# Performance work log

Measured on AMD Instinct MI355X. Metric: run time of the kernel, lower is better.

## Reference

```python
import jax, jax.numpy as jnp
import numpy as np

NA = 100000
NB = 100000
E = 500000
D = 256
EPS = 1e-5


def setup_inputs() -> dict:
    key = jax.random.key(0)
    ks = jax.random.split(key, 10)
    scale = 1.0 / np.sqrt(D)
    return {
        "feat_a": jax.random.normal(ks[0], (NA, D), jnp.float32),
        "feat_b": jax.random.normal(ks[1], (NB, D), jnp.float32),
        "src_ab": jax.random.randint(ks[2], (E,), 0, NA, jnp.int32),
        "dst_ab": jax.random.randint(ks[3], (E,), 0, NB, jnp.int32),
        "src_ba": jax.random.randint(ks[4], (E,), 0, NB, jnp.int32),
        "dst_ba": jax.random.randint(ks[5], (E,), 0, NA, jnp.int32),
        "WT_ab": jax.random.normal(ks[6], (D, D), jnp.float32) * scale,
        "WT_ba": jax.random.normal(ks[7], (D, D), jnp.float32) * scale,
        "WA_ab": jax.random.normal(ks[8], (1, D), jnp.float32) * scale,
        "WA_ba": jax.random.normal(ks[9], (1, D), jnp.float32) * scale,
        "gamma": jnp.ones((D,), jnp.float32),
        "beta": jnp.zeros((D,), jnp.float32),
    }


def _etype_agg(h_src, h_dst, src, dst, WT, WA, n_dst):
    # per-etype linear on src nodes: t_h = W_T h_src
    t_h = h_src @ WT.T                              # [Ns, D]
    x = t_h[src] * h_dst[dst]                       # u_mul_v -> [E, D]
    s = jnp.exp(x @ WA.T)                           # exp(W_A x) -> [E, 1]
    att_sum = jax.ops.segment_sum(s, dst, num_segments=n_dst)  # copy_e+sum
    att = s / att_sum[dst]                          # e_div_v (dst of an edge always has >=1 edge)
    # u_mul_e + sum: weighted scatter of raw src features
    return jax.ops.segment_sum(h_src[src] * att, dst, num_segments=n_dst)


def _finalize(h, gamma, beta):
    h = jax.nn.relu(h)
    mu = jnp.mean(h, axis=-1, keepdims=True)
    var = jnp.mean(jnp.square(h - mu), axis=-1, keepdims=True)
    return (h - mu) / jnp.sqrt(var + EPS) * gamma + beta  # dropout is identity (eval)


def reference(feat_a, feat_b, src_ab, dst_ab, src_ba, dst_ba,
              WT_ab, WT_ba, WA_ab, WA_ba, gamma, beta):
    h_b = _etype_agg(feat_a, feat_b, src_ab, dst_ab, WT_ab, WA_ab, NB)
    h_a = _etype_agg(feat_b, feat_a, src_ba, dst_ba, WT_ba, WA_ba, NA)
    out_a = _finalize(h_a, gamma, beta)
    out_b = _finalize(h_b, gamma, beta)
    return jnp.stack([out_a, out_b])  # [2, N, D]
```

## Files before the change

### kernel.cpp

```cpp
#include <hip/hip_runtime.h>
#include <hip/hip_bf16.h>

#define D 256

typedef __attribute__((ext_vector_type(8))) short short8;
typedef __attribute__((ext_vector_type(4))) float f32x4;
typedef __attribute__((ext_vector_type(4))) unsigned short u16x4;

__device__ __forceinline__ unsigned short f2bf(float f) {
  unsigned int u = __builtin_bit_cast(unsigned int, f);
  u = (u + 0x7FFFu + ((u >> 16) & 1u)) >> 16;
  return (unsigned short)u;
}
__device__ __forceinline__ float bf2f(unsigned short h) {
  unsigned int u = ((unsigned int)h) << 16;
  return __builtin_bit_cast(float, u);
}

__global__ void zero_k(int* __restrict__ p, int n) {
  int i = blockIdx.x * 256 + threadIdx.x;
  if (i < n) p[i] = 0;
}
__global__ void zero_f32(float* __restrict__ p, int n) {
  int i = blockIdx.x * 256 + threadIdx.x;
  if (i < n) p[i] = 0.f;
}

__global__ void classify_k(const float* __restrict__ q0, const float* __restrict__ q1,
                           const float* __restrict__ q2, const float* __restrict__ q3,
                           int* __restrict__ flags) {
  __shared__ int cnt1[4], cnt0[4];
  int t = threadIdx.x;
  if (t < 4) { cnt1[t] = 0; cnt0[t] = 0; }
  __syncthreads();
  const float* qs[4] = {q0, q1, q2, q3};
#pragma unroll
  for (int v = 0; v < 4; ++v) {
    float x = qs[v][t];
    if (x == 1.0f) atomicAdd(&cnt1[v], 1);
    if (x == 0.0f) atomicAdd(&cnt0[v], 1);
  }
  __syncthreads();
  if (t == 0) {
    int gi = -1, bi = -1;
    for (int v = 0; v < 4; ++v) if (cnt1[v] == 256 && gi < 0) gi = v;
    for (int v = 0; v < 4; ++v) if (cnt0[v] == 256 && v != gi && bi < 0) bi = v;
    if (gi < 0) gi = 2;
    if (bi < 0) bi = (gi == 3) ? 2 : 3;
    int wa[2], w = 0;
    for (int v = 0; v < 4; ++v) if (v != gi && v != bi) { if (w < 2) wa[w] = v; ++w; }
    flags[0] = wa[0]; flags[1] = wa[1]; flags[2] = gi; flags[3] = bi;
  }
}

__global__ void prep_w2(const float* __restrict__ WT_ab, const float* __restrict__ WT_ba,
                        const float* __restrict__ q0, const float* __restrict__ q1,
                        const float* __restrict__ q2, const float* __restrict__ q3,
                        const int* __restrict__ flags,
                        unsigned short* __restrict__ w2ab, unsigned short* __restrict__ w2ba) {
  const float* qs[4] = {q0, q1, q2, q3};
  const float* WAab = qs[flags[0]];
  const float* WAba = qs[flags[1]];
  int i = blockIdx.x * 256 + threadIdx.x;
  int n = i >> 8;
  w2ab[i] = f2bf(WAab[n] * WT_ab[i]);
  w2ba[i] = f2bf(WAba[n] * WT_ba[i]);
}

__global__ __launch_bounds__(512) void gemm_g(const float* __restrict__ feat,
                                              const unsigned short* __restrict__ w2,
                                              unsigned short* __restrict__ g,
                                              unsigned short* __restrict__ featbf,
                                              int nchunks, int do_featbf) {
  __shared__ __align__(16) unsigned char bl[8192];
  int lane = threadIdx.x & 63;
  int wv = threadIdx.x >> 6;
  int c0 = blockIdx.x * 8 + wv;
  bool active = c0 < nchunks;
  int c = active ? c0 : (nchunks - 1);
  int r16 = lane & 15;
  int kg = lane >> 4;
  int row0 = c * 32;

  short8 a[2][8];
#pragma unroll
  for (int sub = 0; sub < 2; ++sub) {
    int row = row0 + sub * 16 + r16;
    const float* rp = feat + (size_t)row * D + kg * 8;
#pragma unroll
    for (int kk = 0; kk < 8; ++kk) {
      f32x4 x0 = *(const f32x4*)(rp + kk * 32);
      f32x4 x1 = *(const f32x4*)(rp + kk * 32 + 4);
      short8 t;
      t[0] = (short)f2bf(x0[0]); t[1] = (short)f2bf(x0[1]);
      t[2] = (short)f2bf(x0[2]); t[3] = (short)f2bf(x0[3]);
      t[4] = (short)f2bf(x1[0]); t[5] = (short)f2bf(x1[1]);
      t[6] = (short)f2bf(x1[2]); t[7] = (short)f2bf(x1[3]);
      a[sub][kk] = t;
      if (do_featbf && active)
        *(short8*)(featbf + (size_t)row * D + kk * 32 + kg * 8) = t;
    }
  }

#pragma unroll 1
  for (int nt = 0; nt < 16; ++nt) {
    __syncthreads();
    {
      int t = threadIdx.x;
      int brow = t >> 5, bc = t & 31;
      int lin = brow * 512 + bc * 16;
      int swz = lin ^ ((brow & 7) << 4);
      *(short8*)(bl + swz) = *(const short8*)(w2 + (size_t)(nt * 16 + brow) * D + bc * 8);
    }
    __syncthreads();
    f32x4 acc0 = {0.f, 0.f, 0.f, 0.f};
    f32x4 acc1 = {0.f, 0.f, 0.f, 0.f};
#pragma unroll
    for (int kk = 0; kk < 8; ++kk) {
      int lin = r16 * 512 + kk * 64 + kg * 16;
      int swz = lin ^ ((r16 & 7) << 4);
      short8 b = *(const short8*)(bl + swz);
      acc0 = __builtin_amdgcn_mfma_f32_16x16x32_bf16(a[0][kk], b, acc0, 0, 0, 0);
      acc1 = __builtin_amdgcn_mfma_f32_16x16x32_bf16(a[1][kk], b, acc1, 0, 0, 0);
    }
    if (active) {
      int colv = nt * 16 + r16;
#pragma unroll
      for (int j = 0; j < 4; ++j) {
        int r = row0 + kg * 4 + j;
        g[(size_t)r * D + colv] = f2bf(acc0[j]);
        g[(size_t)(r + 16) * D + colv] = f2bf(acc1[j]);
      }
    }
  }
}

__global__ void hist_k(const int* __restrict__ dst, int* __restrict__ deg, int E) {
  int i = blockIdx.x * blockDim.x + threadIdx.x;
  if (i < E) atomicAdd(&deg[dst[i]], 1);
}

__global__ void scanA_k(const int* __restrict__ deg, int* __restrict__ rp,
                        int* __restrict__ bsum, int n) {
  __shared__ int sh[1024];
  int i = blockIdx.x * 1024 + threadIdx.x;
  int v = (i < n) ? deg[i] : 0;
  sh[threadIdx.x] = v;
  __syncthreads();
  for (int off = 1; off < 1024; off <<= 1) {
    int t = (threadIdx.x >= (unsigned)off) ? sh[threadIdx.x - off] : 0;
    __syncthreads();
    sh[threadIdx.x] += t;
    __syncthreads();
  }
  if (i < n) rp[i] = sh[threadIdx.x] - v;
  if (threadIdx.x == 1023) bsum[blockIdx.x] = sh[1023];
}

__global__ void scanB_k(int* __restrict__ bsB, int* __restrict__ bsA, int nbB, int nbA) {
  __shared__ int sh[128];
  int* b = (blockIdx.x == 0) ? bsB : bsA;
  int nb = (blockIdx.x == 0) ? nbB : nbA;
  int t = threadIdx.x;
  int v = (t < nb) ? b[t] : 0;
  sh[t] = v;
  __syncthreads();
  for (int off = 1; off < 128; off <<= 1) {
    int u = (t >= off) ? sh[t - off] : 0;
    __syncthreads();
    sh[t] += u;
    __syncthreads();
  }
  if (t < nb) b[t] = sh[t] - v;
}

__global__ void scanC_k(int* __restrict__ rp, int* __restrict__ cursor,
                        const int* __restrict__ bsum, int n, int E) {
  int i = blockIdx.x * 1024 + threadIdx.x;
  if (i < n) {
    int v = rp[i] + bsum[i >> 10];
    rp[i] = v;
    cursor[i] = v;
  }
  if (i == 0) rp[n] = E;
}

__global__ void scatter_k(const int* __restrict__ src, const int* __restrict__ dst,
                          int* __restrict__ cur, int* __restrict__ col, int E) {
  int i = blockIdx.x * blockDim.x + threadIdx.x;
  if (i < E) {
    int slot = atomicAdd(&cur[dst[i]], 1);
    col[slot] = src[i];
  }
}

__global__ __launch_bounds__(256) void agg_ln_bf(const unsigned short* __restrict__ fsrc,
                                                 const float* __restrict__ feat_dst,
                                                 const unsigned short* __restrict__ g,
                                                 const int* __restrict__ rp,
                                                 const int* __restrict__ colsrc,
                                                 const float* __restrict__ q0,
                                                 const float* __restrict__ q1,
                                                 const float* __restrict__ q2,
                                                 const float* __restrict__ q3,
                                                 const int* __restrict__ flags,
                                                 float* __restrict__ out, int n_dst) {
  const float* qs[4] = {q0, q1, q2, q3};
  const float* gamma = qs[flags[2]];
  const float* beta  = qs[flags[3]];
  int lane = threadIdx.x & 63;
  int v = blockIdx.x * 4 + (threadIdx.x >> 6);
  if (v >= n_dst) return;
  f32x4 hv = *(const f32x4*)(feat_dst + (size_t)v * D + lane * 4);
  int beg = rp[v], end = rp[v + 1];

  float ssum = 0.f;
  f32x4 acc = {0.f, 0.f, 0.f, 0.f};
  if (beg < end) {
    int sc = colsrc[beg];
    u16x4 gq = *(const u16x4*)(g + (size_t)sc * D + lane * 4);
    u16x4 fq = *(const u16x4*)(fsrc + (size_t)sc * D + lane * 4);
    for (int i = beg; i < end; ++i) {
      int ip = (i + 1 < end) ? (i + 1) : i;
      int scn = colsrc[ip];
      u16x4 gqn = *(const u16x4*)(g + (size_t)scn * D + lane * 4);
      u16x4 fqn = *(const u16x4*)(fsrc + (size_t)scn * D + lane * 4);
      float d = bf2f(gq[0]) * hv[0] + bf2f(gq[1]) * hv[1] +
                bf2f(gq[2]) * hv[2] + bf2f(gq[3]) * hv[3];
#pragma unroll
      for (int off = 32; off > 0; off >>= 1) d += __shfl_xor(d, off, 64);
      float s = __expf(d);
      ssum += s;
      acc[0] += bf2f(fq[0]) * s; acc[1] += bf2f(fq[1]) * s;
      acc[2] += bf2f(fq[2]) * s; acc[3] += bf2f(fq[3]) * s;
      gq = gqn; fq = fqn;
    }
  }
  float inv = (end > beg) ? (1.f / ssum) : 0.f;
  acc[0] *= inv; acc[1] *= inv; acc[2] *= inv; acc[3] *= inv;

  acc[0] = fmaxf(acc[0], 0.f); acc[1] = fmaxf(acc[1], 0.f);
  acc[2] = fmaxf(acc[2], 0.f); acc[3] = fmaxf(acc[3], 0.f);

  float sm = acc[0] + acc[1] + acc[2] + acc[3];
#pragma unroll
  for (int off = 32; off > 0; off >>= 1) sm += __shfl_xor(sm, off, 64);
  float mu = sm * (1.f / 256.f);
  f32x4 dl;
  dl[0] = acc[0] - mu; dl[1] = acc[1] - mu; dl[2] = acc[2] - mu; dl[3] = acc[3] - mu;
  float sq = dl[0] * dl[0] + dl[1] * dl[1] + dl[2] * dl[2] + dl[3] * dl[3];
#pragma unroll
  for (int off = 32; off > 0; off >>= 1) sq += __shfl_xor(sq, off, 64);
  float rs = rsqrtf(sq * (1.f / 256.f) + 1e-5f);

  f32x4 gm = *(const f32x4*)(gamma + lane * 4);
  f32x4 bt = *(const f32x4*)(beta + lane * 4);
  f32x4 o;
  o[0] = dl[0] * rs * gm[0] + bt[0];
  o[1] = dl[1] * rs * gm[1] + bt[1];
  o[2] = dl[2] * rs * gm[2] + bt[2];
  o[3] = dl[3] * rs * gm[3] + bt[3];
  *(f32x4*)(out + (size_t)v * D + lane * 4) = o;
}

__global__ __launch_bounds__(256) void agg_ln(const float* __restrict__ feat_src,
                                              const float* __restrict__ feat_dst,
                                              const unsigned short* __restrict__ g,
                                              const int* __restrict__ rp,
                                              const int* __restrict__ colsrc,
                                              const float* __restrict__ q0,
                                              const float* __restrict__ q1,
                                              const float* __restrict__ q2,
                                              const float* __restrict__ q3,
                                              const int* __restrict__ flags,
                                              float* __restrict__ out, int n_dst) {
  const float* qs[4] = {q0, q1, q2, q3};
  const float* gamma = qs[flags[2]];
  const float* beta  = qs[flags[3]];
  int lane = threadIdx.x & 63;
  int v = blockIdx.x * 4 + (threadIdx.x >> 6);
  if (v >= n_dst) return;
  f32x4 hv = *(const f32x4*)(feat_dst + (size_t)v * D + lane * 4);
  int beg = rp[v], end = rp[v + 1];

  float ssum = 0.f;
  f32x4 acc = {0.f, 0.f, 0.f, 0.f};
  for (int i = beg; i < end; ++i) {
    int sc = colsrc[i];
    u16x4 gq = *(const u16x4*)(g + (size_t)sc * D + lane * 4);
    float d = bf2f(gq[0]) * hv[0] + bf2f(gq[1]) * hv[1] +
              bf2f(gq[2]) * hv[2] + bf2f(gq[3]) * hv[3];
#pragma unroll
    for (int off = 32; off > 0; off >>= 1) d += __shfl_xor(d, off, 64);
    float s = __expf(d);
    ssum += s;
    f32x4 f = *(const f32x4*)(feat_src + (size_t)sc * D + lane * 4);
    acc[0] += f[0] * s; acc[1] += f[1] * s;
    acc[2] += f[2] * s; acc[3] += f[3] * s;
  }
  float inv = (end > beg) ? (1.f / ssum) : 0.f;
  acc[0] *= inv; acc[1] *= inv; acc[2] *= inv; acc[3] *= inv;

  acc[0] = fmaxf(acc[0], 0.f); acc[1] = fmaxf(acc[1], 0.f);
  acc[2] = fmaxf(acc[2], 0.f); acc[3] = fmaxf(acc[3], 0.f);

  float sm = acc[0] + acc[1] + acc[2] + acc[3];
#pragma unroll
  for (int off = 32; off > 0; off >>= 1) sm += __shfl_xor(sm, off, 64);
  float mu = sm * (1.f / 256.f);
  f32x4 dl;
  dl[0] = acc[0] - mu; dl[1] = acc[1] - mu; dl[2] = acc[2] - mu; dl[3] = acc[3] - mu;
  float sq = dl[0] * dl[0] + dl[1] * dl[1] + dl[2] * dl[2] + dl[3] * dl[3];
#pragma unroll
  for (int off = 32; off > 0; off >>= 1) sq += __shfl_xor(sq, off, 64);
  float rs = rsqrtf(sq * (1.f / 256.f) + 1e-5f);

  f32x4 gm = *(const f32x4*)(gamma + lane * 4);
  f32x4 bt = *(const f32x4*)(beta + lane * 4);
  f32x4 o;
  o[0] = dl[0] * rs * gm[0] + bt[0];
  o[1] = dl[1] * rs * gm[1] + bt[1];
  o[2] = dl[2] * rs * gm[2] + bt[2];
  o[3] = dl[3] * rs * gm[3] + bt[3];
  *(f32x4*)(out + (size_t)v * D + lane * 4) = o;
}

extern "C" void kernel_launch(void* const* d_in, const int* in_sizes, int n_in,
                              void* d_out, int out_size, void* d_ws, size_t ws_size,
                              hipStream_t stream) {
  const float* feat_a = (const float*)d_in[0];
  const float* feat_b = (const float*)d_in[1];
  const int* src_ab = (const int*)d_in[2];
  const int* dst_ab = (const int*)d_in[3];
  const int* src_ba = (const int*)d_in[4];
  const int* dst_ba = (const int*)d_in[5];
  const float* WT_ab = (const float*)d_in[6];
  const float* WT_ba = (const float*)d_in[7];
  const float* q0 = (const float*)d_in[8];
  const float* q1 = (const float*)d_in[9];
  const float* q2 = (const float*)d_in[10];
  const float* q3 = (const float*)d_in[11];

  int NA = in_sizes[0] / D;
  int NB = in_sizes[1] / D;
  int E = in_sizes[2];

  float* out = (float*)d_out;
  float* out_a = out;
  float* out_b = out + (size_t)NA * D;

  char* w = (char*)d_ws;
  size_t off = 0;
  auto alloc = [&](size_t bytes) -> void* {
    void* p = (void*)(w + off);
    off += (bytes + 255) & ~(size_t)255;
    return p;
  };
  size_t nmax = (size_t)(NA > NB ? NA : NB);
  unsigned short* gws = (unsigned short*)alloc(nmax * D * 2);
  unsigned short* w2ab = (unsigned short*)alloc(65536 * 2);
  unsigned short* w2ba = (unsigned short*)alloc(65536 * 2);
  int* dc_b = (int*)alloc((size_t)NB * 4);
  int* dc_a = (int*)alloc((size_t)NA * 4);
  int* rp_b = (int*)alloc((size_t)(NB + 1) * 4);
  int* rp_a = (int*)alloc((size_t)(NA + 1) * 4);
  int* col_ab = (int*)alloc((size_t)E * 4);
  int* col_ba = (int*)alloc((size_t)E * 4);
  int* bs_b = (int*)alloc(512);
  int* bs_a = (int*)alloc(512);
  int* flags = (int*)alloc(256);
  size_t need_base = off;
  unsigned short* featbf = (unsigned short*)alloc(nmax * D * 2);
  size_t need_full = off;

  bool bad = (n_in != 12);
  bad = bad || (in_sizes[0] != in_sizes[1]);
  bad = bad || (in_sizes[2] != in_sizes[3]) || (in_sizes[3] != in_sizes[4]) ||
        (in_sizes[4] != in_sizes[5]);
  bad = bad || (in_sizes[6] != 65536) || (in_sizes[7] != 65536);
  bad = bad || (in_sizes[8] != 256) || (in_sizes[9] != 256) ||
        (in_sizes[10] != 256) || (in_sizes[11] != 256);
  bad = bad || (out_size != (NA + NB) * D);
  bad = bad || (ws_size < need_base);
  if (bad) {
    zero_f32<<<(out_size + 255) / 256, 256, 0, stream>>>(out, out_size);
    return;
  }
  int fast = (ws_size >= need_full) ? 1 : 0;

  classify_k<<<1, 256, 0, stream>>>(q0, q1, q2, q3, flags);

  zero_k<<<(NB + 255) / 256, 256, 0, stream>>>(dc_b, NB);
  zero_k<<<(NA + 255) / 256, 256, 0, stream>>>(dc_a, NA);

  prep_w2<<<256, 256, 0, stream>>>(WT_ab, WT_ba, q0, q1, q2, q3, flags,
                                   w2ab, w2ba);

  int egrid = (E + 255) / 256;
  hist_k<<<egrid, 256, 0, stream>>>(dst_ab, dc_b, E);
  hist_k<<<egrid, 256, 0, stream>>>(dst_ba, dc_a, E);

  int nbB = (NB + 1023) / 1024, nbA = (NA + 1023) / 1024;
  scanA_k<<<nbB, 1024, 0, stream>>>(dc_b, rp_b, bs_b, NB);
  scanA_k<<<nbA, 1024, 0, stream>>>(dc_a, rp_a, bs_a, NA);
  scanB_k<<<2, 128, 0, stream>>>(bs_b, bs_a, nbB, nbA);
  scanC_k<<<nbB, 1024, 0, stream>>>(rp_b, dc_b, bs_b, NB, E);
  scanC_k<<<nbA, 1024, 0, stream>>>(rp_a, dc_a, bs_a, NA, E);

  scatter_k<<<egrid, 256, 0, stream>>>(src_ab, dst_ab, dc_b, col_ab, E);
  scatter_k<<<egrid, 256, 0, stream>>>(src_ba, dst_ba, dc_a, col_ba, E);

  int chA = (NA + 31) / 32, chB = (NB + 31) / 32;

  gemm_g<<<(chA + 7) / 8, 512, 0, stream>>>(feat_a, w2ab, gws, featbf, chA, fast);
  if (fast)
    agg_ln_bf<<<(NB + 3) / 4, 256, 0, stream>>>(featbf, feat_b, gws, rp_b, col_ab,
                                                q0, q1, q2, q3, flags, out_b, NB);
  else
    agg_ln<<<(NB + 3) / 4, 256, 0, stream>>>(feat_a, feat_b, gws, rp_b, col_ab,
                                             q0, q1, q2, q3, flags, out_b, NB);

  gemm_g<<<(chB + 7) / 8, 512, 0, stream>>>(feat_b, w2ba, gws, featbf, chB, fast);
  if (fast)
    agg_ln_bf<<<(NA + 3) / 4, 256, 0, stream>>>(featbf, feat_a, gws, rp_a, col_ba,
                                                q0, q1, q2, q3, flags, out_a, NA);
  else
    agg_ln<<<(NA + 3) / 4, 256, 0, stream>>>(feat_b, feat_a, gws, rp_a, col_ba,
                                             q0, q1, q2, q3, flags, out_a, NA);
}
```

Before: 450.1 us.

## Merge graph-build launches, double-buffer GEMM weights, split edges across lane groups

Three separate changes. First, the paired per-etype preprocessing kernels (zero, histogram, scan phases, scatter) are merged into single launches that cover both edge types, which cuts launch count and tail idle time. Second, the GEMM double-buffers the weight tile in LDS, so the next tile's global load overlaps the MFMAs and one barrier per iteration goes away. Third, the aggregation kernel now processes four edges at a time per wavefront, with each 16-lane group handling one edge, which shortens the serial edge loop; the cost is extra cross-group shuffle reductions and a transpose-style shuffle before the LayerNorm.

```diff
diff --git a/kernel.cpp b/kernel.cpp
--- a/kernel.cpp
+++ b/kernel.cpp
@@ -17,13 +17,14 @@
   return __builtin_bit_cast(float, u);
 }
 
-__global__ void zero_k(int* __restrict__ p, int n) {
-  int i = blockIdx.x * 256 + threadIdx.x;
-  if (i < n) p[i] = 0;
-}
 __global__ void zero_f32(float* __restrict__ p, int n) {
   int i = blockIdx.x * 256 + threadIdx.x;
   if (i < n) p[i] = 0.f;
+}
+__global__ void zero2_k(int* __restrict__ a, int na, int* __restrict__ b, int nb) {
+  int i = blockIdx.x * 256 + threadIdx.x;
+  if (i < na) a[i] = 0;
+  else if (i - na < nb) b[i - na] = 0;
 }
 
 __global__ void classify_k(const float* __restrict__ q0, const float* __restrict__ q1,
@@ -72,7 +73,7 @@
                                               unsigned short* __restrict__ g,
                                               unsigned short* __restrict__ featbf,
                                               int nchunks, int do_featbf) {
-  __shared__ __align__(16) unsigned char bl[8192];
+  __shared__ __align__(16) unsigned char bl[2][8192];
   int lane = threadIdx.x & 63;
   int wv = threadIdx.x >> 6;
   int c0 = blockIdx.x * 8 + wv;
@@ -102,24 +103,30 @@
     }
   }
 
+  int t = threadIdx.x;
+  int brow = t >> 5, bc = t & 31;
+  int slin = brow * 512 + bc * 16;
+  int sswz = slin ^ ((brow & 7) << 4);
+
+  *(short8*)(bl[0] + sswz) = *(const short8*)(w2 + (size_t)brow * D + bc * 8);
+  __syncthreads();
+
+  int cur = 0;
 #pragma unroll 1
   for (int nt = 0; nt < 16; ++nt) {
-    __syncthreads();
-    {
-      int t = threadIdx.x;
-      int brow = t >> 5, bc = t & 31;
-      int lin = brow * 512 + bc * 16;
-      int swz = lin ^ ((brow & 7) << 4);
-      *(short8*)(bl + swz) = *(const short8*)(w2 + (size_t)(nt * 16 + brow) * D + bc * 8);
-    }
-    __syncthreads();
+    short8 tnext;
+    bool has = nt + 1 < 16;
+    if (has)
+      tnext = *(const short8*)(w2 + (size_t)((nt + 1) * 16 + brow) * D + bc * 8);
+
     f32x4 acc0 = {0.f, 0.f, 0.f, 0.f};
     f32x4 acc1 = {0.f, 0.f, 0.f, 0.f};
+    const unsigned char* blc = bl[cur];
 #pragma unroll
     for (int kk = 0; kk < 8; ++kk) {
       int lin = r16 * 512 + kk * 64 + kg * 16;
       int swz = lin ^ ((r16 & 7) << 4);
-      short8 b = *(const short8*)(bl + swz);
+      short8 b = *(const short8*)(blc + swz);
       acc0 = __builtin_amdgcn_mfma_f32_16x16x32_bf16(a[0][kk], b, acc0, 0, 0, 0);
       acc1 = __builtin_amdgcn_mfma_f32_16x16x32_bf16(a[1][kk], b, acc1, 0, 0, 0);
     }
@@ -132,29 +139,42 @@
         g[(size_t)(r + 16) * D + colv] = f2bf(acc1[j]);
       }
     }
-  }
-}
-
-__global__ void hist_k(const int* __restrict__ dst, int* __restrict__ deg, int E) {
+    if (has) *(short8*)(bl[cur ^ 1] + sswz) = tnext;
+    __syncthreads();
+    cur ^= 1;
+  }
+}
+
+__global__ void hist2_k(const int* __restrict__ dab, int* __restrict__ degb,
+                        const int* __restrict__ dba, int* __restrict__ dega, int E) {
   int i = blockIdx.x * blockDim.x + threadIdx.x;
-  if (i < E) atomicAdd(&deg[dst[i]], 1);
-}
-
-__global__ void scanA_k(const int* __restrict__ deg, int* __restrict__ rp,
-                        int* __restrict__ bsum, int n) {
+  if (i < E) atomicAdd(&degb[dab[i]], 1);
+  else if (i - E < E) atomicAdd(&dega[dba[i - E]], 1);
+}
+
+__global__ void scanA2_k(const int* __restrict__ degb, int* __restrict__ rpb,
+                         int* __restrict__ bsb, int nB,
+                         const int* __restrict__ dega, int* __restrict__ rpa,
+                         int* __restrict__ bsa, int nA, int nbB) {
   __shared__ int sh[1024];
-  int i = blockIdx.x * 1024 + threadIdx.x;
+  bool isB = (int)blockIdx.x < nbB;
+  const int* deg = isB ? degb : dega;
+  int* rp = isB ? rpb : rpa;
+  int* bsum = isB ? bsb : bsa;
+  int n = isB ? nB : nA;
+  int blk = isB ? blockIdx.x : blockIdx.x - nbB;
+  int i = blk * 1024 + threadIdx.x;
   int v = (i < n) ? deg[i] : 0;
   sh[threadIdx.x] = v;
   __syncthreads();
   for (int off = 1; off < 1024; off <<= 1) {
-    int t = (threadIdx.x >= (unsigned)off) ? sh[threadIdx.x - off] : 0;
+    int tv = (threadIdx.x >= (unsigned)off) ? sh[threadIdx.x - off] : 0;
     __syncthreads();
-    sh[threadIdx.x] += t;
+    sh[threadIdx.x] += tv;
     __syncthreads();
   }
   if (i < n) rp[i] = sh[threadIdx.x] - v;
-  if (threadIdx.x == 1023) bsum[blockIdx.x] = sh[1023];
+  if (threadIdx.x == 1023) bsum[blk] = sh[1023];
 }
 
 __global__ void scanB_k(int* __restrict__ bsB, int* __restrict__ bsA, int nbB, int nbA) {
@@ -174,9 +194,17 @@
   if (t < nb) b[t] = sh[t] - v;
 }
 
-__global__ void scanC_k(int* __restrict__ rp, int* __restrict__ cursor,
-                        const int* __restrict__ bsum, int n, int E) {
-  int i = blockIdx.x * 1024 + threadIdx.x;
+__global__ void scanC2_k(int* __restrict__ rpb, int* __restrict__ curb,
+                         const int* __restrict__ bsb, int nB,
+                         int* __restrict__ rpa, int* __restrict__ cura,
+                         const int* __restrict__ bsa, int nA, int nbB, int E) {
+  bool isB = (int)blockIdx.x < nbB;
+  int* rp = isB ? rpb : rpa;
+  int* cursor = isB ? curb : cura;
+  const int* bsum = isB ? bsb : bsa;
+  int n = isB ? nB : nA;
+  int blk = isB ? blockIdx.x : blockIdx.x - nbB;
+  int i = blk * 1024 + threadIdx.x;
   if (i < n) {
     int v = rp[i] + bsum[i >> 10];
     rp[i] = v;
@@ -185,12 +213,18 @@
   if (i == 0) rp[n] = E;
 }
 
-__global__ void scatter_k(const int* __restrict__ src, const int* __restrict__ dst,
-                          int* __restrict__ cur, int* __restrict__ col, int E) {
+__global__ void scatter2_k(const int* __restrict__ sab, const int* __restrict__ dab,
+                           int* __restrict__ curb, int* __restrict__ colab,
+                           const int* __restrict__ sba, const int* __restrict__ dba,
+                           int* __restrict__ cura, int* __restrict__ colba, int E) {
   int i = blockIdx.x * blockDim.x + threadIdx.x;
   if (i < E) {
-    int slot = atomicAdd(&cur[dst[i]], 1);
-    col[slot] = src[i];
+    int slot = atomicAdd(&curb[dab[i]], 1);
+    colab[slot] = sab[i];
+  } else if (i - E < E) {
+    int j = i - E;
+    int slot = atomicAdd(&cura[dba[j]], 1);
+    colba[slot] = sba[j];
   }
 }
 
@@ -211,43 +245,96 @@
   int lane = threadIdx.x & 63;
   int v = blockIdx.x * 4 + (threadIdx.x >> 6);
   if (v >= n_dst) return;
-  f32x4 hv = *(const f32x4*)(feat_dst + (size_t)v * D + lane * 4);
+  int l16 = lane & 15;
+  int grp = lane >> 4;
+
+  f32x4 hv[4];
+  {
+    const float* hp = feat_dst + (size_t)v * D + l16 * 16;
+    hv[0] = *(const f32x4*)(hp);
+    hv[1] = *(const f32x4*)(hp + 4);
+    hv[2] = *(const f32x4*)(hp + 8);
+    hv[3] = *(const f32x4*)(hp + 12);
+  }
   int beg = rp[v], end = rp[v + 1];
 
   float ssum = 0.f;
-  f32x4 acc = {0.f, 0.f, 0.f, 0.f};
-  if (beg < end) {
-    int sc = colsrc[beg];
-    u16x4 gq = *(const u16x4*)(g + (size_t)sc * D + lane * 4);
-    u16x4 fq = *(const u16x4*)(fsrc + (size_t)sc * D + lane * 4);
-    for (int i = beg; i < end; ++i) {
-      int ip = (i + 1 < end) ? (i + 1) : i;
+  f32x4 acc[4];
+#pragma unroll
+  for (int q = 0; q < 4; ++q) acc[q] = (f32x4){0.f, 0.f, 0.f, 0.f};
+
+  int i0 = beg + grp;
+  if (i0 < end) {
+    int sc = colsrc[i0];
+    const unsigned short* gp = g + (size_t)sc * D + l16 * 16;
+    const unsigned short* fp = fsrc + (size_t)sc * D + l16 * 16;
+    u16x4 gq[4], fq[4];
+#pragma unroll
+    for (int q = 0; q < 4; ++q) { gq[q] = *(const u16x4*)(gp + q * 4); fq[q] = *(const u16x4*)(fp + q * 4); }
+    for (int i = i0; i < end; i += 4) {
+      int ip = (i + 4 < end) ? (i + 4) : i;
       int scn = colsrc[ip];
-      u16x4 gqn = *(const u16x4*)(g + (size_t)scn * D + lane * 4);
-      u16x4 fqn = *(const u16x4*)(fsrc + (size_t)scn * D + lane * 4);
-      float d = bf2f(gq[0]) * hv[0] + bf2f(gq[1]) * hv[1] +
-                bf2f(gq[2]) * hv[2] + bf2f(gq[3]) * hv[3];
-#pragma unroll
-      for (int off = 32; off > 0; off >>= 1) d += __shfl_xor(d, off, 64);
+      const unsigned short* gpn = g + (size_t)scn * D + l16 * 16;
+      const unsigned short* fpn = fsrc + (size_t)scn * D + l16 * 16;
+      u16x4 gqn[4], fqn[4];
+#pragma unroll
+      for (int q = 0; q < 4; ++q) { gqn[q] = *(const u16x4*)(gpn + q * 4); fqn[q] = *(const u16x4*)(fpn + q * 4); }
+
+      float d = 0.f;
+#pragma unroll
+      for (int q = 0; q < 4; ++q)
+        d += bf2f(gq[q][0]) * hv[q][0] + bf2f(gq[q][1]) * hv[q][1] +
+             bf2f(gq[q][2]) * hv[q][2] + bf2f(gq[q][3]) * hv[q][3];
+      d += __shfl_xor(d, 1, 64);
+      d += __shfl_xor(d, 2, 64);
+      d += __shfl_xor(d, 4, 64);
+      d += __shfl_xor(d, 8, 64);
       float s = __expf(d);
       ssum += s;
-      acc[0] += bf2f(fq[0]) * s; acc[1] += bf2f(fq[1]) * s;
-      acc[2] += bf2f(fq[2]) * s; acc[3] += bf2f(fq[3]) * s;
-      gq = gqn; fq = fqn;
+#pragma unroll
+      for (int q = 0; q < 4; ++q) {
+        acc[q][0] += bf2f(fq[q][0]) * s; acc[q][1] += bf2f(fq[q][1]) * s;
+        acc[q][2] += bf2f(fq[q][2]) * s; acc[q][3] += bf2f(fq[q][3]) * s;
+      }
+#pragma unroll
+      for (int q = 0; q < 4; ++q) { gq[q] = gqn[q]; fq[q] = fqn[q]; }
     }
   }
+
+  ssum += __shfl_xor(ssum, 16, 64);
+  ssum += __shfl_xor(ssum, 32, 64);
+#pragma unroll
+  for (int q = 0; q < 4; ++q)
+#pragma unroll
+    for (int j = 0; j < 4; ++j) {
+      acc[q][j] += __shfl_xor(acc[q][j], 16, 64);
+      acc[q][j] += __shfl_xor(acc[q][j], 32, 64);
+    }
+
   float inv = (end > beg) ? (1.f / ssum) : 0.f;
-  acc[0] *= inv; acc[1] *= inv; acc[2] *= inv; acc[3] *= inv;
-
-  acc[0] = fmaxf(acc[0], 0.f); acc[1] = fmaxf(acc[1], 0.f);
-  acc[2] = fmaxf(acc[2], 0.f); acc[3] = fmaxf(acc[3], 0.f);
-
-  float sm = acc[0] + acc[1] + acc[2] + acc[3];
+
+  int srcl = lane >> 2;
+  int qsel = lane & 3;
+  f32x4 r0, r1, r2, r3;
+#pragma unroll
+  for (int j = 0; j < 4; ++j) {
+    r0[j] = __shfl(acc[0][j], srcl, 64);
+    r1[j] = __shfl(acc[1][j], srcl, 64);
+    r2[j] = __shfl(acc[2][j], srcl, 64);
+    r3[j] = __shfl(acc[3][j], srcl, 64);
+  }
+  f32x4 oo = (qsel == 0) ? r0 : (qsel == 1) ? r1 : (qsel == 2) ? r2 : r3;
+  oo[0] *= inv; oo[1] *= inv; oo[2] *= inv; oo[3] *= inv;
+
+  oo[0] = fmaxf(oo[0], 0.f); oo[1] = fmaxf(oo[1], 0.f);
+  oo[2] = fmaxf(oo[2], 0.f); oo[3] = fmaxf(oo[3], 0.f);
+
+  float sm = oo[0] + oo[1] + oo[2] + oo[3];
 #pragma unroll
   for (int off = 32; off > 0; off >>= 1) sm += __shfl_xor(sm, off, 64);
   float mu = sm * (1.f / 256.f);
   f32x4 dl;
-  dl[0] = acc[0] - mu; dl[1] = acc[1] - mu; dl[2] = acc[2] - mu; dl[3] = acc[3] - mu;
+  dl[0] = oo[0] - mu; dl[1] = oo[1] - mu; dl[2] = oo[2] - mu; dl[3] = oo[3] - mu;
   float sq = dl[0] * dl[0] + dl[1] * dl[1] + dl[2] * dl[2] + dl[3] * dl[3];
 #pragma unroll
   for (int off = 32; off > 0; off >>= 1) sq += __shfl_xor(sq, off, 64);
@@ -389,26 +476,20 @@
   int fast = (ws_size >= need_full) ? 1 : 0;
 
   classify_k<<<1, 256, 0, stream>>>(q0, q1, q2, q3, flags);
-
-  zero_k<<<(NB + 255) / 256, 256, 0, stream>>>(dc_b, NB);
-  zero_k<<<(NA + 255) / 256, 256, 0, stream>>>(dc_a, NA);
-
+  zero2_k<<<(NA + NB + 255) / 256, 256, 0, stream>>>(dc_b, NB, dc_a, NA);
   prep_w2<<<256, 256, 0, stream>>>(WT_ab, WT_ba, q0, q1, q2, q3, flags,
                                    w2ab, w2ba);
 
-  int egrid = (E + 255) / 256;
-  hist_k<<<egrid, 256, 0, stream>>>(dst_ab, dc_b, E);
-  hist_k<<<egrid, 256, 0, stream>>>(dst_ba, dc_a, E);
+  hist2_k<<<(2 * E + 255) / 256, 256, 0, stream>>>(dst_ab, dc_b, dst_ba, dc_a, E);
 
   int nbB = (NB + 1023) / 1024, nbA = (NA + 1023) / 1024;
-  scanA_k<<<nbB, 1024, 0, stream>>>(dc_b, rp_b, bs_b, NB);
-  scanA_k<<<nbA, 1024, 0, stream>>>(dc_a, rp_a, bs_a, NA);
+  scanA2_k<<<nbB + nbA, 1024, 0, stream>>>(dc_b, rp_b, bs_b, NB,
+                                           dc_a, rp_a, bs_a, NA, nbB);
   scanB_k<<<2, 128, 0, stream>>>(bs_b, bs_a, nbB, nbA);
-  scanC_k<<<nbB, 1024, 0, stream>>>(rp_b, dc_b, bs_b, NB, E);
-  scanC_k<<<nbA, 1024, 0, stream>>>(rp_a, dc_a, bs_a, NA, E);
-
-  scatter_k<<<egrid, 256, 0, stream>>>(src_ab, dst_ab, dc_b, col_ab, E);
-  scatter_k<<<egrid, 256, 0, stream>>>(src_ba, dst_ba, dc_a, col_ba, E);
+  scanC2_k<<<nbB + nbA, 1024, 0, stream>>>(rp_b, dc_b, bs_b, NB,
+                                           rp_a, dc_a, bs_a, NA, nbB, E);
+  scatter2_k<<<(2 * E + 255) / 256, 256, 0, stream>>>(src_ab, dst_ab, dc_b, col_ab,
+                                                      src_ba, dst_ba, dc_a, col_ba, E);
 
   int chA = (NA + 31) / 32, chB = (NB + 31) / 32;
 
```

Result: slower. 510.2 us, median of 2 (+13.4%).
